# Kernel tuning notes

Measured on AMD Instinct MI355X. Metric: run time of the kernel, lower is better.

The kernel has to match this reference:

```python
import jax, jax.numpy as jnp
import numpy as np

EPS = 1e-6
NH, DK, DV = 4, 32, 32

def _ln2d(x, w, b):
    # LayerNorm2d: normalize over channel dim (dim=1), biased variance
    mu = jnp.mean(x, axis=1, keepdims=True)
    var = jnp.mean((x - mu) ** 2, axis=1, keepdims=True)
    y = (x - mu) / jnp.sqrt(var + EPS)
    return w[None, :, None, None] * y + b[None, :, None, None]

def _c1x1(w, x):
    # 1x1 conv == per-pixel matmul: w [out,in], x [B,C,H,W]
    return jnp.einsum('oc,bchw->bohw', w, x)

def _shifts(x, r):
    # All (2r+1)^2 zero-padded spatial shifts, row-major (dy,dx) like nn.Unfold.
    B, C, H, W = x.shape
    xp = jnp.pad(x, ((0, 0), (0, 0), (r, r), (r, r)))
    return jnp.stack([xp[:, :, dy:dy + H, dx:dx + W]
                      for dy in range(2 * r + 1) for dx in range(2 * r + 1)], axis=0)

def _local_attn(q, k, v, kernel):
    # Correlation-pyramid local attention: per-pixel q.k over kxk window of k,
    # softmax over window (temperature sqrt(d_k)), weighted sum of v window
    # (weights shared across channels, per ChannelAttention).
    B, _, H, W = q.shape
    r = (kernel - 1) // 2
    K2 = kernel * kernel
    qh = q.reshape(B, NH, DK, H, W)
    ks = _shifts(k, r).reshape(K2, B, NH, DK, H, W)
    corr = jnp.einsum('bncyx,jbncyx->jbnyx', qh, ks)            # [K2,B,NH,H,W]
    attn = jax.nn.softmax(corr / jnp.sqrt(jnp.float32(DK)), axis=0)
    vs = _shifts(v, r).reshape(K2, B, NH, DV, H, W)
    out = jnp.einsum('jbnyx,jbncyx->bncyx', attn, vs)
    return out.reshape(B, NH * DV, H, W)

def _mha(q, k, v, kernel, wq, wk, wv, fc, lnw, lnb):
    resid = q
    heads = _local_attn(_c1x1(wq, q), _c1x1(wk, k), _c1x1(wv, v), kernel)
    out = _c1x1(fc, heads) + resid   # residual BEFORE LN (per source)
    return _ln2d(out, lnw, lnb)

def _ffn(x, w1, b1, w2, b2, lnw, lnb):
    h = jax.nn.relu(_c1x1(w1, x) + b1[None, :, None, None])
    y = _c1x1(w2, h) + b2[None, :, None, None]
    return _ln2d(y, lnw, lnb) + x    # LN BEFORE residual add (per source)

def setup_inputs():
    key = jax.random.key(0)
    ks = jax.random.split(key, 24)
    B, C, H, W = 4, 128, 96, 96
    s = (2.0 / C) ** 0.5
    f = jnp.float32
    return {
        'input1': jax.random.normal(ks[0], (B, C, H, W), f),
        'input2': jax.random.normal(ks[1], (B, C, H, W), f),
        'wq_s': jax.random.normal(ks[2], (NH * DK, C), f) * s,
        'wk_s': jax.random.normal(ks[3], (NH * DK, C), f) * s,
        'wv_s': jax.random.normal(ks[4], (NH * DV, C), f) * s,
        'fc_s': jax.random.normal(ks[5], (C, NH * DV), f) * s,
        'lnw_s': jnp.ones((C,), f),
        'lnb_s': jnp.zeros((C,), f),
        'wq_c': jax.random.normal(ks[6], (NH * DK, C), f) * s,
        'wk_c': jax.random.normal(ks[7], (NH * DK, C), f) * s,
        'wv_c': jax.random.normal(ks[8], (NH * DV, C), f) * s,
        'fc_c': jax.random.normal(ks[9], (C, NH * DV), f) * s,
        'lnw_c': jnp.ones((C,), f),
        'lnb_c': jnp.zeros((C,), f),
        'w1': jax.random.normal(ks[10], (C, C), f) * s,
        'b1': jnp.zeros((C,), f),
        'w2': jax.random.normal(ks[11], (C, C), f) * s,
        'b2': jnp.zeros((C,), f),
        'lnw_f': jnp.ones((C,), f),
        'lnb_f': jnp.zeros((C,), f),
        'kernel': 5,
        'pad': 2,
    }

def reference(input1, input2, wq_s, wk_s, wv_s, fc_s, lnw_s, lnb_s,
              wq_c, wk_c, wv_c, fc_c, lnw_c, lnb_c,
              w1, b1, w2, b2, lnw_f, lnb_f, kernel, pad):
    slf1 = _mha(input1, input1, input1, kernel, wq_s, wk_s, wv_s, fc_s, lnw_s, lnb_s)
    slf2 = _mha(input2, input2, input2, kernel, wq_s, wk_s, wv_s, fc_s, lnw_s, lnb_s)
    crs1 = _mha(slf1, slf2, slf2, kernel, wq_c, wk_c, wv_c, fc_c, lnw_c, lnb_c)
    crs2 = _mha(slf2, slf1, slf1, kernel, wq_c, wk_c, wv_c, fc_c, lnw_c, lnb_c)
    out1 = _ffn(crs1, w1, b1, w2, b2, lnw_f, lnb_f)
    out2 = _ffn(crs2, w1, b1, w2, b2, lnw_f, lnb_f)
    return (out1, out2)
```

## Files before the change

### kernel.cpp

```cpp
#include <hip/hip_runtime.h>
#include <hip/hip_bf16.h>

typedef _Float16 h16;
typedef __attribute__((ext_vector_type(8))) _Float16 f16x8v;
typedef __attribute__((ext_vector_type(2))) _Float16 h2v;
typedef __attribute__((ext_vector_type(4))) float f32x4;
#define DI __device__ __forceinline__

constexpr int CH = 128;
constexpr int HH = 96, WW = 96;
constexpr int HW = HH * WW;
constexpr int NB = 4;
constexpr int NPIX = NB * HW;
constexpr int LDT = 136;
constexpr size_t HP = (size_t)NPIX * 32;
constexpr int GH = NPIX / 64;
constexpr int TY = 4, TX = 32;
constexpr int HYH = TY + 4, HXH = TX + 4;
constexpr int LDC = 40;
constexpr int ATB = NPIX / (TY * TX) * 4;

struct __attribute__((aligned(16))) h16x8 { h16 h[8]; };
struct Set { h16 *q, *k, *v; };

DI float h2f(h16 x) { return (float)x; }
DI h16   f2h(float x) { return (h16)x; }


DI void stage_x_cl(const h16* __restrict__ src, int ldx, h16* xl, int t) {
    #pragma unroll
    for (int i = 0; i < 4; ++i) {
        int id = t + 256 * i, px = id >> 4, cc = (id & 15) * 8;
        *reinterpret_cast<f16x8v*>(&xl[px * LDT + cc]) =
            *reinterpret_cast<const f16x8v*>(&src[(size_t)px * ldx + cc]);
    }
}

DI void stage_x_pl(const float* __restrict__ src, h16* xl, int t) {
    #pragma unroll
    for (int i = 0; i < 8; ++i) {
        int id = t + 256 * i, c = id >> 4, p4 = (id & 15) * 4;
        float4 v = *reinterpret_cast<const float4*>(&src[(size_t)c * HW + p4]);
        xl[(p4 + 0) * LDT + c] = f2h(v.x);
        xl[(p4 + 1) * LDT + c] = f2h(v.y);
        xl[(p4 + 2) * LDT + c] = f2h(v.z);
        xl[(p4 + 3) * LDT + c] = f2h(v.w);
    }
}

DI void stage_x_hm(const h16* __restrict__ Tq, h16* xl, int p0, int t) {
    const int px = t >> 2, c8 = (t & 3) * 8;
    #pragma unroll
    for (int h = 0; h < 4; ++h)
        *reinterpret_cast<f16x8v*>(&xl[px * LDT + h * 32 + c8]) =
            *reinterpret_cast<const f16x8v*>(&Tq[(size_t)h * HP + (size_t)(p0 + px) * 32 + c8]);
}

DI void stage_w(const float* __restrict__ w, h16* wl, int t) {
    #pragma unroll
    for (int i = 0; i < 8; ++i) {
        int id = t + 256 * i, o = id >> 4, cc = (id & 15) * 8;
        float4 a = *reinterpret_cast<const float4*>(&w[o * CH + cc]);
        float4 b = *reinterpret_cast<const float4*>(&w[o * CH + cc + 4]);
        h16x8 tmp;
        tmp.h[0] = f2h(a.x); tmp.h[1] = f2h(a.y); tmp.h[2] = f2h(a.z); tmp.h[3] = f2h(a.w);
        tmp.h[4] = f2h(b.x); tmp.h[5] = f2h(b.y); tmp.h[6] = f2h(b.z); tmp.h[7] = f2h(b.w);
        *reinterpret_cast<f16x8v*>(&wl[o * LDT + cc]) = *reinterpret_cast<const f16x8v*>(&tmp);
    }
}

DI void gemm64(const h16* xl, const h16* wl, int w, int l, f32x4* acc) {
    const int s = l & 15, g = l >> 4;
    #pragma unroll
    for (int ks = 0; ks < 4; ++ks) {
        f16x8v a = *reinterpret_cast<const f16x8v*>(&xl[(16 * w + s) * LDT + ks * 32 + g * 8]);
        #pragma unroll
        for (int n = 0; n < 8; ++n) {
            f16x8v b = *reinterpret_cast<const f16x8v*>(&wl[(16 * n + s) * LDT + ks * 32 + g * 8]);
            acc[n] = __builtin_amdgcn_mfma_f32_16x16x32_f16(a, b, acc[n], 0, 0, 0);
        }
    }
}

DI void qkv_epi(const f32x4* acc, h16* comp, int p0, int w, int l) {
    const int s = l & 15, g = l >> 4;
    #pragma unroll
    for (int n = 0; n < 8; ++n) {
        const int o = 16 * n + s, head = o >> 5, ch = o & 31;
        h16* pl = comp + (size_t)head * HP;
        #pragma unroll
        for (int j = 0; j < 4; ++j) {
            int px = 16 * w + 4 * g + j;
            pl[(size_t)(p0 + px) * 32 + ch] = f2h(acc[n][j]);
        }
    }
}

__global__ __launch_bounds__(256, 2)
void qkv_self_b(const float* __restrict__ x0, const float* __restrict__ x1,
                const float* __restrict__ w0, const float* __restrict__ w1_,
                const float* __restrict__ w2_, Set sA, Set sB) {
    __shared__ h16 xl[64 * LDT];
    __shared__ h16 wl[CH * LDT];
    const int bid = blockIdx.x, half = bid / GH, p0 = (bid % GH) * 64;
    const float* xv = half ? x1 : x0;
    Set S = half ? sB : sA;
    const int t = threadIdx.x;
    const int b = p0 / HW, hw0 = p0 % HW;
    stage_x_pl(xv + (size_t)b * CH * HW + hw0, xl, t);
    const int w = t >> 6, l = t & 63;
    #pragma unroll
    for (int m = 0; m < 3; ++m) {
        const float* wm = (m == 0) ? w0 : ((m == 1) ? w1_ : w2_);
        h16* comp = (m == 0) ? S.q : ((m == 1) ? S.k : S.v);
        __syncthreads();
        stage_w(wm, wl, t);
        __syncthreads();
        f32x4 acc[8];
        #pragma unroll
        for (int n = 0; n < 8; ++n) acc[n] = {0.f, 0.f, 0.f, 0.f};
        gemm64(xl, wl, w, l, acc);
        qkv_epi(acc, comp, p0, w, l);
    }
}

__global__ __launch_bounds__(256, 2)
void qkv_cross_b(const h16* __restrict__ xa, const h16* __restrict__ xb,
                 const float* __restrict__ wq, const float* __restrict__ wk,
                 const float* __restrict__ wv, Set c1, Set c2) {
    __shared__ h16 xl[64 * LDT];
    __shared__ h16 wl[CH * LDT];
    const int bid = blockIdx.x, half = bid / GH, p0 = (bid % GH) * 64;
    const h16* xq  = half ? xb : xa;
    const h16* xkv = half ? xa : xb;
    Set S = half ? c2 : c1;
    const int t = threadIdx.x;
    const int w = t >> 6, l = t & 63;

    stage_x_cl(xq + (size_t)p0 * CH, CH, xl, t);
    stage_w(wq, wl, t);
    __syncthreads();
    {
        f32x4 acc[8];
        #pragma unroll
        for (int n = 0; n < 8; ++n) acc[n] = {0.f, 0.f, 0.f, 0.f};
        gemm64(xl, wl, w, l, acc);
        qkv_epi(acc, S.q, p0, w, l);
    }
    __syncthreads();
    stage_x_cl(xkv + (size_t)p0 * CH, CH, xl, t);
    stage_w(wk, wl, t);
    __syncthreads();
    {
        f32x4 acc[8];
        #pragma unroll
        for (int n = 0; n < 8; ++n) acc[n] = {0.f, 0.f, 0.f, 0.f};
        gemm64(xl, wl, w, l, acc);
        qkv_epi(acc, S.k, p0, w, l);
    }
    __syncthreads();
    stage_w(wv, wl, t);
    __syncthreads();
    {
        f32x4 acc[8];
        #pragma unroll
        for (int n = 0; n < 8; ++n) acc[n] = {0.f, 0.f, 0.f, 0.f};
        gemm64(xl, wl, w, l, acc);
        qkv_epi(acc, S.v, p0, w, l);
    }
}

__global__ __launch_bounds__(256)
void attn5b(Set s0, Set s1) {
    __shared__ h16 kv[HYH * HXH * LDC];
    const int bid = blockIdx.x, setId = bid / ATB, id = bid - setId * ATB;
    Set S = setId ? s1 : s0;
    const int n = id & 3, tile = id >> 2;
    const int img = tile / 72, rem = tile % 72, tr = rem / 3, tc = rem % 3;
    const int y0 = tr * TY, x0 = tc * TX;
    const int t = threadIdx.x;
    const int p = t >> 1, half = t & 1, ch16 = half * 16;
    const int ty = p >> 5, tx = p & 31;
    h16* Qh = S.q + (size_t)n * HP;
    const h16* Kh = S.k + (size_t)n * HP;
    const h16* Vh = S.v + (size_t)n * HP;
    const int gp = img * HW + (y0 + ty) * WW + (x0 + tx);
    h16* qp = Qh + (size_t)gp * 32 + ch16;

    f16x8v q0 = *reinterpret_cast<const f16x8v*>(qp);
    f16x8v q1 = *reinterpret_cast<const f16x8v*>(qp + 8);
    {
        const h16 sc = (h16)0.17677669529663689f;
        #pragma unroll
        for (int e = 0; e < 8; ++e) { q0[e] *= sc; q1[e] *= sc; }
    }

    #pragma unroll
    for (int i = 0; i < 5; ++i) {
        int id2 = t + 256 * i;
        if (id2 < 1152) {
            int r = id2 / 144, c = id2 - r * 144, px = c >> 2, c8 = (c & 3) * 8;
            int y = y0 + r - 2, x = x0 + px - 2;
            f16x8v v = {0, 0, 0, 0, 0, 0, 0, 0};
            if ((unsigned)y < (unsigned)HH && (unsigned)x < (unsigned)WW)
                v = *reinterpret_cast<const f16x8v*>(&Kh[((size_t)(img * HW + y * WW + x)) * 32 + c8]);
            *reinterpret_cast<f16x8v*>(&kv[(r * HXH + px) * LDC + c8]) = v;
        }
    }
    __syncthreads();

    float corr[25];
    #pragma unroll
    for (int dy = 0; dy < 5; ++dy)
        #pragma unroll
        for (int dx = 0; dx < 5; ++dx) {
            const h16* kp = &kv[((ty + dy) * HXH + tx + dx) * LDC + ch16];
            f16x8v k0 = *reinterpret_cast<const f16x8v*>(kp);
            f16x8v k1 = *reinterpret_cast<const f16x8v*>(kp + 8);
            float s;
#if __has_builtin(__builtin_amdgcn_fdot2)
            s = __builtin_amdgcn_fdot2(h2v{q0[0], q0[1]}, h2v{k0[0], k0[1]}, 0.f, false);
            s = __builtin_amdgcn_fdot2(h2v{q0[2], q0[3]}, h2v{k0[2], k0[3]}, s, false);
            s = __builtin_amdgcn_fdot2(h2v{q0[4], q0[5]}, h2v{k0[4], k0[5]}, s, false);
            s = __builtin_amdgcn_fdot2(h2v{q0[6], q0[7]}, h2v{k0[6], k0[7]}, s, false);
            s = __builtin_amdgcn_fdot2(h2v{q1[0], q1[1]}, h2v{k1[0], k1[1]}, s, false);
            s = __builtin_amdgcn_fdot2(h2v{q1[2], q1[3]}, h2v{k1[2], k1[3]}, s, false);
            s = __builtin_amdgcn_fdot2(h2v{q1[4], q1[5]}, h2v{k1[4], k1[5]}, s, false);
            s = __builtin_amdgcn_fdot2(h2v{q1[6], q1[7]}, h2v{k1[6], k1[7]}, s, false);
#else
            s = 0.f;
            #pragma unroll
            for (int e = 0; e < 8; ++e) s += h2f(q0[e]) * h2f(k0[e]);
            #pragma unroll
            for (int e = 0; e < 8; ++e) s += h2f(q1[e]) * h2f(k1[e]);
#endif
            s += __shfl_xor(s, 1);
            corr[dy * 5 + dx] = s;
        }

    float m = corr[0];
    #pragma unroll
    for (int j = 1; j < 25; ++j) m = fmaxf(m, corr[j]);
    float sum = 0.f;
    #pragma unroll
    for (int j = 0; j < 25; ++j) {
        float e = __expf(corr[j] - m);
        corr[j] = e; sum += e;
    }
    const float inv = 1.f / sum;

    __syncthreads();
    #pragma unroll
    for (int i = 0; i < 5; ++i) {
        int id2 = t + 256 * i;
        if (id2 < 1152) {
            int r = id2 / 144, c = id2 - r * 144, px = c >> 2, c8 = (c & 3) * 8;
            int y = y0 + r - 2, x = x0 + px - 2;
            f16x8v v = {0, 0, 0, 0, 0, 0, 0, 0};
            if ((unsigned)y < (unsigned)HH && (unsigned)x < (unsigned)WW)
                v = *reinterpret_cast<const f16x8v*>(&Vh[((size_t)(img * HW + y * WW + x)) * 32 + c8]);
            *reinterpret_cast<f16x8v*>(&kv[(r * HXH + px) * LDC + c8]) = v;
        }
    }
    __syncthreads();

    f16x8v o0 = {0, 0, 0, 0, 0, 0, 0, 0};
    f16x8v o1 = {0, 0, 0, 0, 0, 0, 0, 0};
    #pragma unroll
    for (int dy = 0; dy < 5; ++dy)
        #pragma unroll
        for (int dx = 0; dx < 5; ++dx) {
            const h16 ah = f2h(corr[dy * 5 + dx]);
            const f16x8v av = {ah, ah, ah, ah, ah, ah, ah, ah};
            const h16* vp = &kv[((ty + dy) * HXH + tx + dx) * LDC + ch16];
            f16x8v v0 = *reinterpret_cast<const f16x8v*>(vp);
            f16x8v v1 = *reinterpret_cast<const f16x8v*>(vp + 8);
            o0 += av * v0;
            o1 += av * v1;
        }
    {
        const h16 ih = f2h(inv);
        const f16x8v iv = {ih, ih, ih, ih, ih, ih, ih, ih};
        o0 *= iv; o1 *= iv;
    }
    *reinterpret_cast<f16x8v*>(qp)     = o0;
    *reinterpret_cast<f16x8v*>(qp + 8) = o1;
}

template<bool RPLANAR>
__global__ __launch_bounds__(256, 2)
void fcln_b(const h16* __restrict__ t0, const h16* __restrict__ t1,
            const void* __restrict__ r0, const void* __restrict__ r1,
            const float* __restrict__ wfc, const float* __restrict__ gamma,
            const float* __restrict__ beta, h16* __restrict__ o0,
            h16* __restrict__ o1) {
    __shared__ h16 xl[64 * LDT];
    __shared__ h16 wl[CH * LDT];
    const int bid = blockIdx.x, half = bid / GH, p0 = (bid % GH) * 64;
    const h16* tin = half ? t1 : t0;
    const void* residv = half ? r1 : r0;
    h16* out = half ? o1 : o0;
    const int t = threadIdx.x;
    stage_x_hm(tin, xl, p0, t);
    stage_w(wfc, wl, t);
    __syncthreads();
    const int w = t >> 6, l = t & 63, s = l & 15, g = l >> 4;
    f32x4 acc[8];
    #pragma unroll
    for (int n = 0; n < 8; ++n) acc[n] = {0.f, 0.f, 0.f, 0.f};
    gemm64(xl, wl, w, l, acc);

    const int b = p0 / HW, hw0 = p0 % HW;
    float r[8][4];
    #pragma unroll
    for (int n = 0; n < 8; ++n) {
        const int o = 16 * n + s;
        #pragma unroll
        for (int j = 0; j < 4; ++j) {
            const int px = 16 * w + 4 * g + j;
            float rv;
            if (RPLANAR)
                rv = ((const float*)residv)[(size_t)b * CH * HW + (size_t)o * HW + hw0 + px];
            else
                rv = h2f(((const h16*)residv)[(size_t)(p0 + px) * CH + o]);
            r[n][j] = acc[n][j] + rv;
        }
    }
    float gm[8], bt[8];
    #pragma unroll
    for (int n = 0; n < 8; ++n) { gm[n] = gamma[16 * n + s]; bt[n] = beta[16 * n + s]; }
    #pragma unroll
    for (int j = 0; j < 4; ++j) {
        float sm = 0.f, sq = 0.f;
        #pragma unroll
        for (int n = 0; n < 8; ++n) { float v = r[n][j]; sm += v; sq += v * v; }
        sm += __shfl_xor(sm, 1); sq += __shfl_xor(sq, 1);
        sm += __shfl_xor(sm, 2); sq += __shfl_xor(sq, 2);
        sm += __shfl_xor(sm, 4); sq += __shfl_xor(sq, 4);
        sm += __shfl_xor(sm, 8); sq += __shfl_xor(sq, 8);
        const float mu = sm * (1.f / 128.f);
        const float var = sq * (1.f / 128.f) - mu * mu;
        const float rs = rsqrtf(var + 1e-6f);
        const int px = 16 * w + 4 * g + j;
        #pragma unroll
        for (int n = 0; n < 8; ++n) {
            const int o = 16 * n + s;
            out[(size_t)(p0 + px) * CH + o] = f2h(gm[n] * (r[n][j] - mu) * rs + bt[n]);
        }
    }
}

__global__ __launch_bounds__(256, 2)
void ffn_fused(const h16* __restrict__ y0, const h16* __restrict__ y1,
               const float* __restrict__ w1m, const float* __restrict__ b1v,
               const float* __restrict__ w2m, const float* __restrict__ b2v,
               const float* __restrict__ gamma, const float* __restrict__ beta,
               float* __restrict__ o0, float* __restrict__ o1) {
    __shared__ __align__(16) char smem[64 * LDT * 2 * 2 + CH * LDT * 2];
    h16*   xl = (h16*)smem;
    h16*   hl = (h16*)(smem + 64 * LDT * 2);
    h16*   wl = (h16*)(smem + 64 * LDT * 2 * 2);
    float* ll = (float*)(smem + 64 * LDT * 2 * 2);
    const int bid = blockIdx.x, half = bid / GH, p0 = (bid % GH) * 64;
    const h16* y = half ? y1 : y0;
    float* outp = half ? o1 : o0;
    const int t = threadIdx.x;
    stage_x_cl(y + (size_t)p0 * CH, CH, xl, t);
    stage_w(w1m, wl, t);
    __syncthreads();
    const int w = t >> 6, l = t & 63, s = l & 15, g = l >> 4;
    f32x4 acc[8];
    #pragma unroll
    for (int n = 0; n < 8; ++n) acc[n] = {0.f, 0.f, 0.f, 0.f};
    gemm64(xl, wl, w, l, acc);
    #pragma unroll
    for (int n = 0; n < 8; ++n) {
        const int o = 16 * n + s;
        const float bv = b1v[o];
        #pragma unroll
        for (int j = 0; j < 4; ++j) {
            const int px = 16 * w + 4 * g + j;
            hl[px * LDT + o] = f2h(fmaxf(acc[n][j] + bv, 0.f));
        }
    }
    __syncthreads();
    stage_w(w2m, wl, t);
    __syncthreads();
    f32x4 acc2[8];
    #pragma unroll
    for (int n = 0; n < 8; ++n) acc2[n] = {0.f, 0.f, 0.f, 0.f};
    gemm64(hl, wl, w, l, acc2);

    float gm[8], bt[8], r[8][4];
    #pragma unroll
    for (int n = 0; n < 8; ++n) {
        const int o = 16 * n + s;
        gm[n] = gamma[o]; bt[n] = beta[o];
        const float bv = b2v[o];
        #pragma unroll
        for (int j = 0; j < 4; ++j) r[n][j] = acc2[n][j] + bv;
    }
    float val[8][4];
    #pragma unroll
    for (int j = 0; j < 4; ++j) {
        float sm = 0.f, sq = 0.f;
        #pragma unroll
        for (int n = 0; n < 8; ++n) { float v = r[n][j]; sm += v; sq += v * v; }
        sm += __shfl_xor(sm, 1); sq += __shfl_xor(sq, 1);
        sm += __shfl_xor(sm, 2); sq += __shfl_xor(sq, 2);
        sm += __shfl_xor(sm, 4); sq += __shfl_xor(sq, 4);
        sm += __shfl_xor(sm, 8); sq += __shfl_xor(sq, 8);
        const float mu = sm * (1.f / 128.f);
        const float var = sq * (1.f / 128.f) - mu * mu;
        const float rs = rsqrtf(var + 1e-6f);
        const int px = 16 * w + 4 * g + j;
        #pragma unroll
        for (int n = 0; n < 8; ++n) {
            const int o = 16 * n + s;
            val[n][j] = gm[n] * (r[n][j] - mu) * rs + bt[n]
                      + h2f(xl[px * LDT + o]);
        }
    }
    __syncthreads();
    #pragma unroll
    for (int n = 0; n < 8; ++n) {
        const int o = 16 * n + s;
        #pragma unroll
        for (int j = 0; j < 4; ++j) ll[o * 65 + 16 * w + 4 * g + j] = val[n][j];
    }
    __syncthreads();
    const int b = p0 / HW, hw0 = p0 % HW;
    #pragma unroll
    for (int i = 0; i < 8; ++i) {
        int id = t + 256 * i, c = id >> 4, p4 = (id & 15) * 4;
        float4 v = { ll[c * 65 + p4], ll[c * 65 + p4 + 1],
                     ll[c * 65 + p4 + 2], ll[c * 65 + p4 + 3] };
        *reinterpret_cast<float4*>(&outp[(size_t)b * CH * HW + (size_t)c * HW + hw0 + p4]) = v;
    }
}

extern "C" void kernel_launch(void* const* d_in, const int* in_sizes, int n_in,
                              void* d_out, int out_size, void* d_ws, size_t ws_size,
                              hipStream_t stream) {
    (void)in_sizes; (void)n_in; (void)out_size; (void)ws_size;
    const float* in1  = (const float*)d_in[0];
    const float* in2  = (const float*)d_in[1];
    const float* wq_s = (const float*)d_in[2];
    const float* wk_s = (const float*)d_in[3];
    const float* wv_s = (const float*)d_in[4];
    const float* fc_s = (const float*)d_in[5];
    const float* lnw_s= (const float*)d_in[6];
    const float* lnb_s= (const float*)d_in[7];
    const float* wq_c = (const float*)d_in[8];
    const float* wk_c = (const float*)d_in[9];
    const float* wv_c = (const float*)d_in[10];
    const float* fc_c = (const float*)d_in[11];
    const float* lnw_c= (const float*)d_in[12];
    const float* lnb_c= (const float*)d_in[13];
    const float* w1   = (const float*)d_in[14];
    const float* b1   = (const float*)d_in[15];
    const float* w2   = (const float*)d_in[16];
    const float* b2   = (const float*)d_in[17];
    const float* lnw_f= (const float*)d_in[18];
    const float* lnb_f= (const float*)d_in[19];

    const size_t BUF  = (size_t)NPIX * CH;
    const size_t BUFB = BUF * 2;
    char* ws = (char*)d_ws;
    h16* W0 = (h16*)(ws + 0 * BUFB);
    h16* W1 = (h16*)(ws + 1 * BUFB);
    h16* W2 = (h16*)(ws + 2 * BUFB);
    h16* W3 = (h16*)(ws + 3 * BUFB);
    h16* D0 = (h16*)d_out;
    h16* D1 = (h16*)((char*)d_out + 1 * BUFB);
    h16* D2 = (h16*)((char*)d_out + 2 * BUFB);
    h16* D3 = (h16*)((char*)d_out + 3 * BUFB);
    float* out1 = (float*)d_out;
    float* out2 = (float*)d_out + BUF;

    const dim3 B(256), BA(256);

    Set SA = {W0, W1, W2};
    Set SB = {W3, D0, D1};
    h16* X1 = D2;
    h16* X2 = D3;

    qkv_self_b<<<dim3(2 * GH), B, 0, stream>>>(in1, in2, wq_s, wk_s, wv_s, SA, SB);
    attn5b<<<dim3(2 * ATB), BA, 0, stream>>>(SA, SB);
    fcln_b<true><<<dim3(2 * GH), B, 0, stream>>>(SA.q, SB.q, in1, in2,
                                                 fc_s, lnw_s, lnb_s, X1, X2);

    Set C1 = {W0, W1, W2};
    Set C2 = {W3, D0, D1};
    qkv_cross_b<<<dim3(2 * GH), B, 0, stream>>>(X1, X2, wq_c, wk_c, wv_c, C1, C2);
    attn5b<<<dim3(2 * ATB), BA, 0, stream>>>(C1, C2);
    h16* Y1 = W1;
    h16* Y2 = W2;
    fcln_b<false><<<dim3(2 * GH), B, 0, stream>>>(C1.q, C2.q, X1, X2,
                                                  fc_c, lnw_c, lnb_c, Y1, Y2);

    ffn_fused<<<dim3(2 * GH), B, 0, stream>>>(Y1, Y2, w1, b1, w2, b2,
                                              lnw_f, lnb_f, out1, out2);
}
```

Measured before the change: 162.9 us.

## Fuse self-attn fc+LN into cross QKV projection and cross fc+LN into FFN

Merges the self-attention output projection, residual and LayerNorm with the cross-attention QKV projections into one kernel. Each block processes both streams for its 64 pixels, so the normalized X1/X2 tiles stay in shared memory and feed the Q/K/V GEMMs without a reload. The cross-attention fc+LN is likewise folded into the FFN kernel, cutting the pipeline from seven launches to five and removing global round trips of intermediates. In exchange the fused kernel launches half as many blocks, each with more shared memory and longer serial work, which may lower occupancy and parallelism.

```diff
diff --git a/kernel.cpp b/kernel.cpp
--- a/kernel.cpp
+++ b/kernel.cpp
@@ -93,6 +93,25 @@
             int px = 16 * w + 4 * g + j;
             pl[(size_t)(p0 + px) * 32 + ch] = f2h(acc[n][j]);
         }
+    }
+}
+
+DI void ln128(float r[8][4], const float* gm, const float* bt, float val[8][4]) {
+    #pragma unroll
+    for (int j = 0; j < 4; ++j) {
+        float sm = 0.f, sq = 0.f;
+        #pragma unroll
+        for (int n = 0; n < 8; ++n) { float v = r[n][j]; sm += v; sq += v * v; }
+        sm += __shfl_xor(sm, 1); sq += __shfl_xor(sq, 1);
+        sm += __shfl_xor(sm, 2); sq += __shfl_xor(sq, 2);
+        sm += __shfl_xor(sm, 4); sq += __shfl_xor(sq, 4);
+        sm += __shfl_xor(sm, 8); sq += __shfl_xor(sq, 8);
+        const float mu = sm * (1.f / 128.f);
+        const float var = sq * (1.f / 128.f) - mu * mu;
+        const float rs = rsqrtf(var + 1e-6f);
+        #pragma unroll
+        for (int n = 0; n < 8; ++n)
+            val[n][j] = gm[n] * (r[n][j] - mu) * rs + bt[n];
     }
 }
 
@@ -121,52 +140,6 @@
         for (int n = 0; n < 8; ++n) acc[n] = {0.f, 0.f, 0.f, 0.f};
         gemm64(xl, wl, w, l, acc);
         qkv_epi(acc, comp, p0, w, l);
-    }
-}
-
-__global__ __launch_bounds__(256, 2)
-void qkv_cross_b(const h16* __restrict__ xa, const h16* __restrict__ xb,
-                 const float* __restrict__ wq, const float* __restrict__ wk,
-                 const float* __restrict__ wv, Set c1, Set c2) {
-    __shared__ h16 xl[64 * LDT];
-    __shared__ h16 wl[CH * LDT];
-    const int bid = blockIdx.x, half = bid / GH, p0 = (bid % GH) * 64;
-    const h16* xq  = half ? xb : xa;
-    const h16* xkv = half ? xa : xb;
-    Set S = half ? c2 : c1;
-    const int t = threadIdx.x;
-    const int w = t >> 6, l = t & 63;
-
-    stage_x_cl(xq + (size_t)p0 * CH, CH, xl, t);
-    stage_w(wq, wl, t);
-    __syncthreads();
-    {
-        f32x4 acc[8];
-        #pragma unroll
-        for (int n = 0; n < 8; ++n) acc[n] = {0.f, 0.f, 0.f, 0.f};
-        gemm64(xl, wl, w, l, acc);
-        qkv_epi(acc, S.q, p0, w, l);
-    }
-    __syncthreads();
-    stage_x_cl(xkv + (size_t)p0 * CH, CH, xl, t);
-    stage_w(wk, wl, t);
-    __syncthreads();
-    {
-        f32x4 acc[8];
-        #pragma unroll
-        for (int n = 0; n < 8; ++n) acc[n] = {0.f, 0.f, 0.f, 0.f};
-        gemm64(xl, wl, w, l, acc);
-        qkv_epi(acc, S.k, p0, w, l);
-    }
-    __syncthreads();
-    stage_w(wv, wl, t);
-    __syncthreads();
-    {
-        f32x4 acc[8];
-        #pragma unroll
-        for (int n = 0; n < 8; ++n) acc[n] = {0.f, 0.f, 0.f, 0.f};
-        gemm64(xl, wl, w, l, acc);
-        qkv_epi(acc, S.v, p0, w, l);
     }
 }
 
@@ -287,146 +260,251 @@
     *reinterpret_cast<f16x8v*>(qp + 8) = o1;
 }
 
-template<bool RPLANAR>
 __global__ __launch_bounds__(256, 2)
-void fcln_b(const h16* __restrict__ t0, const h16* __restrict__ t1,
-            const void* __restrict__ r0, const void* __restrict__ r1,
-            const float* __restrict__ wfc, const float* __restrict__ gamma,
-            const float* __restrict__ beta, h16* __restrict__ o0,
-            h16* __restrict__ o1) {
-    __shared__ h16 xl[64 * LDT];
+void fcx_b(const h16* __restrict__ tA, const h16* __restrict__ tB,
+           const float* __restrict__ in1, const float* __restrict__ in2,
+           const float* __restrict__ wfc, const float* __restrict__ gamma,
+           const float* __restrict__ beta,
+           const float* __restrict__ wq, const float* __restrict__ wk,
+           const float* __restrict__ wv,
+           h16* __restrict__ x1g, h16* __restrict__ x2g, Set c1, Set c2) {
+    __shared__ h16 xA[64 * LDT];
+    __shared__ h16 xB[64 * LDT];
     __shared__ h16 wl[CH * LDT];
-    const int bid = blockIdx.x, half = bid / GH, p0 = (bid % GH) * 64;
-    const h16* tin = half ? t1 : t0;
-    const void* residv = half ? r1 : r0;
-    h16* out = half ? o1 : o0;
-    const int t = threadIdx.x;
-    stage_x_hm(tin, xl, p0, t);
+    const int t = threadIdx.x, p0 = blockIdx.x * 64;
+    const int w = t >> 6, l = t & 63, s = l & 15, g4 = l >> 4;
+    const int b = p0 / HW, hw0 = p0 % HW;
+
+    stage_x_hm(tA, xA, p0, t);
+    stage_x_hm(tB, xB, p0, t);
     stage_w(wfc, wl, t);
     __syncthreads();
-    const int w = t >> 6, l = t & 63, s = l & 15, g = l >> 4;
-    f32x4 acc[8];
-    #pragma unroll
-    for (int n = 0; n < 8; ++n) acc[n] = {0.f, 0.f, 0.f, 0.f};
-    gemm64(xl, wl, w, l, acc);
-
-    const int b = p0 / HW, hw0 = p0 % HW;
-    float r[8][4];
+
+    float gm[8], bt[8];
+    #pragma unroll
+    for (int n = 0; n < 8; ++n) { gm[n] = gamma[16 * n + s]; bt[n] = beta[16 * n + s]; }
+
+    h16 vA[8][4], vB[8][4];
+    {
+        f32x4 acc[8];
+        #pragma unroll
+        for (int n = 0; n < 8; ++n) acc[n] = {0.f, 0.f, 0.f, 0.f};
+        gemm64(xA, wl, w, l, acc);
+        float r[8][4], val[8][4];
+        #pragma unroll
+        for (int n = 0; n < 8; ++n) {
+            const int o = 16 * n + s;
+            #pragma unroll
+            for (int j = 0; j < 4; ++j) {
+                const int px = 16 * w + 4 * g4 + j;
+                r[n][j] = acc[n][j] +
+                    in1[(size_t)b * CH * HW + (size_t)o * HW + hw0 + px];
+            }
+        }
+        ln128(r, gm, bt, val);
+        #pragma unroll
+        for (int n = 0; n < 8; ++n)
+            #pragma unroll
+            for (int j = 0; j < 4; ++j) vA[n][j] = f2h(val[n][j]);
+    }
+    {
+        f32x4 acc[8];
+        #pragma unroll
+        for (int n = 0; n < 8; ++n) acc[n] = {0.f, 0.f, 0.f, 0.f};
+        gemm64(xB, wl, w, l, acc);
+        float r[8][4], val[8][4];
+        #pragma unroll
+        for (int n = 0; n < 8; ++n) {
+            const int o = 16 * n + s;
+            #pragma unroll
+            for (int j = 0; j < 4; ++j) {
+                const int px = 16 * w + 4 * g4 + j;
+                r[n][j] = acc[n][j] +
+                    in2[(size_t)b * CH * HW + (size_t)o * HW + hw0 + px];
+            }
+        }
+        ln128(r, gm, bt, val);
+        #pragma unroll
+        for (int n = 0; n < 8; ++n)
+            #pragma unroll
+            for (int j = 0; j < 4; ++j) vB[n][j] = f2h(val[n][j]);
+    }
+    __syncthreads();
     #pragma unroll
     for (int n = 0; n < 8; ++n) {
         const int o = 16 * n + s;
         #pragma unroll
         for (int j = 0; j < 4; ++j) {
-            const int px = 16 * w + 4 * g + j;
-            float rv;
-            if (RPLANAR)
-                rv = ((const float*)residv)[(size_t)b * CH * HW + (size_t)o * HW + hw0 + px];
-            else
-                rv = h2f(((const h16*)residv)[(size_t)(p0 + px) * CH + o]);
-            r[n][j] = acc[n][j] + rv;
-        }
-    }
-    float gm[8], bt[8];
-    #pragma unroll
-    for (int n = 0; n < 8; ++n) { gm[n] = gamma[16 * n + s]; bt[n] = beta[16 * n + s]; }
-    #pragma unroll
-    for (int j = 0; j < 4; ++j) {
-        float sm = 0.f, sq = 0.f;
-        #pragma unroll
-        for (int n = 0; n < 8; ++n) { float v = r[n][j]; sm += v; sq += v * v; }
-        sm += __shfl_xor(sm, 1); sq += __shfl_xor(sq, 1);
-        sm += __shfl_xor(sm, 2); sq += __shfl_xor(sq, 2);
-        sm += __shfl_xor(sm, 4); sq += __shfl_xor(sq, 4);
-        sm += __shfl_xor(sm, 8); sq += __shfl_xor(sq, 8);
-        const float mu = sm * (1.f / 128.f);
-        const float var = sq * (1.f / 128.f) - mu * mu;
-        const float rs = rsqrtf(var + 1e-6f);
-        const int px = 16 * w + 4 * g + j;
-        #pragma unroll
-        for (int n = 0; n < 8; ++n) {
-            const int o = 16 * n + s;
-            out[(size_t)(p0 + px) * CH + o] = f2h(gm[n] * (r[n][j] - mu) * rs + bt[n]);
-        }
+            const int px = 16 * w + 4 * g4 + j;
+            xA[px * LDT + o] = vA[n][j];
+            xB[px * LDT + o] = vB[n][j];
+            x1g[(size_t)(p0 + px) * CH + o] = vA[n][j];
+            x2g[(size_t)(p0 + px) * CH + o] = vB[n][j];
+        }
+    }
+    __syncthreads();
+
+    stage_w(wq, wl, t);
+    __syncthreads();
+    {
+        f32x4 acc[8];
+        #pragma unroll
+        for (int n = 0; n < 8; ++n) acc[n] = {0.f, 0.f, 0.f, 0.f};
+        gemm64(xA, wl, w, l, acc);
+        qkv_epi(acc, c1.q, p0, w, l);
+    }
+    {
+        f32x4 acc[8];
+        #pragma unroll
+        for (int n = 0; n < 8; ++n) acc[n] = {0.f, 0.f, 0.f, 0.f};
+        gemm64(xB, wl, w, l, acc);
+        qkv_epi(acc, c2.q, p0, w, l);
+    }
+    __syncthreads();
+    stage_w(wk, wl, t);
+    __syncthreads();
+    {
+        f32x4 acc[8];
+        #pragma unroll
+        for (int n = 0; n < 8; ++n) acc[n] = {0.f, 0.f, 0.f, 0.f};
+        gemm64(xB, wl, w, l, acc);
+        qkv_epi(acc, c1.k, p0, w, l);
+    }
+    {
+        f32x4 acc[8];
+        #pragma unroll
+        for (int n = 0; n < 8; ++n) acc[n] = {0.f, 0.f, 0.f, 0.f};
+        gemm64(xA, wl, w, l, acc);
+        qkv_epi(acc, c2.k, p0, w, l);
+    }
+    __syncthreads();
+    stage_w(wv, wl, t);
+    __syncthreads();
+    {
+        f32x4 acc[8];
+        #pragma unroll
+        for (int n = 0; n < 8; ++n) acc[n] = {0.f, 0.f, 0.f, 0.f};
+        gemm64(xB, wl, w, l, acc);
+        qkv_epi(acc, c1.v, p0, w, l);
+    }
+    {
+        f32x4 acc[8];
+        #pragma unroll
+        for (int n = 0; n < 8; ++n) acc[n] = {0.f, 0.f, 0.f, 0.f};
+        gemm64(xA, wl, w, l, acc);
+        qkv_epi(acc, c2.v, p0, w, l);
     }
 }
 
 __global__ __launch_bounds__(256, 2)
-void ffn_fused(const h16* __restrict__ y0, const h16* __restrict__ y1,
-               const float* __restrict__ w1m, const float* __restrict__ b1v,
-               const float* __restrict__ w2m, const float* __restrict__ b2v,
-               const float* __restrict__ gamma, const float* __restrict__ beta,
-               float* __restrict__ o0, float* __restrict__ o1) {
+void ffn_ln_b(const h16* __restrict__ t0, const h16* __restrict__ t1,
+              const h16* __restrict__ x0, const h16* __restrict__ x1,
+              const float* __restrict__ wfc, const float* __restrict__ gc,
+              const float* __restrict__ bc,
+              const float* __restrict__ w1m, const float* __restrict__ b1v,
+              const float* __restrict__ w2m, const float* __restrict__ b2v,
+              const float* __restrict__ gf, const float* __restrict__ bf,
+              float* __restrict__ o0, float* __restrict__ o1) {
     __shared__ __align__(16) char smem[64 * LDT * 2 * 2 + CH * LDT * 2];
     h16*   xl = (h16*)smem;
-    h16*   hl = (h16*)(smem + 64 * LDT * 2);
+    h16*   yl = (h16*)(smem + 64 * LDT * 2);
     h16*   wl = (h16*)(smem + 64 * LDT * 2 * 2);
     float* ll = (float*)(smem + 64 * LDT * 2 * 2);
     const int bid = blockIdx.x, half = bid / GH, p0 = (bid % GH) * 64;
-    const h16* y = half ? y1 : y0;
+    const h16* tin = half ? t1 : t0;
+    const h16* xg  = half ? x1 : x0;
     float* outp = half ? o1 : o0;
     const int t = threadIdx.x;
-    stage_x_cl(y + (size_t)p0 * CH, CH, xl, t);
-    stage_w(w1m, wl, t);
-    __syncthreads();
-    const int w = t >> 6, l = t & 63, s = l & 15, g = l >> 4;
-    f32x4 acc[8];
-    #pragma unroll
-    for (int n = 0; n < 8; ++n) acc[n] = {0.f, 0.f, 0.f, 0.f};
-    gemm64(xl, wl, w, l, acc);
+    const int w = t >> 6, l = t & 63, s = l & 15, g4 = l >> 4;
+
+    stage_x_hm(tin, xl, p0, t);
+    stage_w(wfc, wl, t);
+    __syncthreads();
+
+    h16 yv[8][4];
+    {
+        f32x4 acc[8];
+        #pragma unroll
+        for (int n = 0; n < 8; ++n) acc[n] = {0.f, 0.f, 0.f, 0.f};
+        gemm64(xl, wl, w, l, acc);
+        float gm[8], bt[8], r[8][4], val[8][4];
+        #pragma unroll
+        for (int n = 0; n < 8; ++n) { gm[n] = gc[16 * n + s]; bt[n] = bc[16 * n + s]; }
+        #pragma unroll
+        for (int n = 0; n < 8; ++n) {
+            const int o = 16 * n + s;
+            #pragma unroll
+            for (int j = 0; j < 4; ++j) {
+                const int px = 16 * w + 4 * g4 + j;
+                r[n][j] = acc[n][j] + h2f(xg[(size_t)(p0 + px) * CH + o]);
+            }
+        }
+        ln128(r, gm, bt, val);
+        #pragma unroll
+        for (int n = 0; n < 8; ++n)
+            #pragma unroll
+            for (int j = 0; j < 4; ++j) yv[n][j] = f2h(val[n][j]);
+    }
+    __syncthreads();
     #pragma unroll
     for (int n = 0; n < 8; ++n) {
         const int o = 16 * n + s;
-        const float bv = b1v[o];
-        #pragma unroll
-        for (int j = 0; j < 4; ++j) {
-            const int px = 16 * w + 4 * g + j;
-            hl[px * LDT + o] = f2h(fmaxf(acc[n][j] + bv, 0.f));
+        #pragma unroll
+        for (int j = 0; j < 4; ++j)
+            yl[(16 * w + 4 * g4 + j) * LDT + o] = yv[n][j];
+    }
+    stage_w(w1m, wl, t);
+    __syncthreads();
+
+    {
+        f32x4 acc[8];
+        #pragma unroll
+        for (int n = 0; n < 8; ++n) acc[n] = {0.f, 0.f, 0.f, 0.f};
+        gemm64(yl, wl, w, l, acc);
+        #pragma unroll
+        for (int n = 0; n < 8; ++n) {
+            const int o = 16 * n + s;
+            const float bv = b1v[o];
+            #pragma unroll
+            for (int j = 0; j < 4; ++j)
+                xl[(16 * w + 4 * g4 + j) * LDT + o] = f2h(fmaxf(acc[n][j] + bv, 0.f));
         }
     }
     __syncthreads();
     stage_w(w2m, wl, t);
     __syncthreads();
-    f32x4 acc2[8];
-    #pragma unroll
-    for (int n = 0; n < 8; ++n) acc2[n] = {0.f, 0.f, 0.f, 0.f};
-    gemm64(hl, wl, w, l, acc2);
-
-    float gm[8], bt[8], r[8][4];
+
+    float val[8][4];
+    {
+        f32x4 acc[8];
+        #pragma unroll
+        for (int n = 0; n < 8; ++n) acc[n] = {0.f, 0.f, 0.f, 0.f};
+        gemm64(xl, wl, w, l, acc);
+        float gm[8], bt[8], r[8][4];
+        #pragma unroll
+        for (int n = 0; n < 8; ++n) { gm[n] = gf[16 * n + s]; bt[n] = bf[16 * n + s]; }
+        #pragma unroll
+        for (int n = 0; n < 8; ++n) {
+            const int o = 16 * n + s;
+            const float bv = b2v[o];
+            #pragma unroll
+            for (int j = 0; j < 4; ++j) r[n][j] = acc[n][j] + bv;
+        }
+        ln128(r, gm, bt, val);
+        #pragma unroll
+        for (int n = 0; n < 8; ++n) {
+            const int o = 16 * n + s;
+            #pragma unroll
+            for (int j = 0; j < 4; ++j)
+                val[n][j] += h2f(yl[(16 * w + 4 * g4 + j) * LDT + o]);
+        }
+    }
+    __syncthreads();
     #pragma unroll
     for (int n = 0; n < 8; ++n) {
         const int o = 16 * n + s;
-        gm[n] = gamma[o]; bt[n] = beta[o];
-        const float bv = b2v[o];
-        #pragma unroll
-        for (int j = 0; j < 4; ++j) r[n][j] = acc2[n][j] + bv;
-    }
-    float val[8][4];
-    #pragma unroll
-    for (int j = 0; j < 4; ++j) {
-        float sm = 0.f, sq = 0.f;
-        #pragma unroll
-        for (int n = 0; n < 8; ++n) { float v = r[n][j]; sm += v; sq += v * v; }
-        sm += __shfl_xor(sm, 1); sq += __shfl_xor(sq, 1);
-        sm += __shfl_xor(sm, 2); sq += __shfl_xor(sq, 2);
-        sm += __shfl_xor(sm, 4); sq += __shfl_xor(sq, 4);
-        sm += __shfl_xor(sm, 8); sq += __shfl_xor(sq, 8);
-        const float mu = sm * (1.f / 128.f);
-        const float var = sq * (1.f / 128.f) - mu * mu;
-        const float rs = rsqrtf(var + 1e-6f);
-        const int px = 16 * w + 4 * g + j;
-        #pragma unroll
-        for (int n = 0; n < 8; ++n) {
-            const int o = 16 * n + s;
-            val[n][j] = gm[n] * (r[n][j] - mu) * rs + bt[n]
-                      + h2f(xl[px * LDT + o]);
-        }
-    }
-    __syncthreads();
-    #pragma unroll
-    for (int n = 0; n < 8; ++n) {
-        const int o = 16 * n + s;
-        #pragma unroll
-        for (int j = 0; j < 4; ++j) ll[o * 65 + 16 * w + 4 * g + j] = val[n][j];
+        #pragma unroll
+        for (int j = 0; j < 4; ++j) ll[o * 65 + 16 * w + 4 * g4 + j] = val[n][j];
     }
     __syncthreads();
     const int b = p0 / HW, hw0 = p0 % HW;
@@ -478,27 +556,23 @@
     float* out1 = (float*)d_out;
     float* out2 = (float*)d_out + BUF;
 
-    const dim3 B(256), BA(256);
-
-    Set SA = {W0, W1, W2};
-    Set SB = {W3, D0, D1};
-    h16* X1 = D2;
-    h16* X2 = D3;
+    const dim3 B(256);
+
+    Set SA = {W0, D0, D1};
+    Set SB = {W1, D2, D3};
+    h16* X1 = W2;
+    h16* X2 = W3;
+    Set C1 = {W0, D0, D1};
+    Set C2 = {W1, D2, D3};
 
     qkv_self_b<<<dim3(2 * GH), B, 0, stream>>>(in1, in2, wq_s, wk_s, wv_s, SA, SB);
-    attn5b<<<dim3(2 * ATB), BA, 0, stream>>>(SA, SB);
-    fcln_b<true><<<dim3(2 * GH), B, 0, stream>>>(SA.q, SB.q, in1, in2,
-                                                 fc_s, lnw_s, lnb_s, X1, X2);
-
-    Set C1 = {W0, W1, W2};
-    Set C2 = {W3, D0, D1};
-    qkv_cross_b<<<dim3(2 * GH), B, 0, stream>>>(X1, X2, wq_c, wk_c, wv_c, C1, C2);
-    attn5b<<<dim3(2 * ATB), BA, 0, stream>>>(C1, C2);
-    h16* Y1 = W1;
-    h16* Y2 = W2;
-    fcln_b<false><<<dim3(2 * GH), B, 0, stream>>>(C1.q, C2.q, X1, X2,
-                                                  fc_c, lnw_c, lnb_c, Y1, Y2);
-
-    ffn_fused<<<dim3(2 * GH), B, 0, stream>>>(Y1, Y2, w1, b1, w2, b2,
-                                              lnw_f, lnb_f, out1, out2);
-}
+    attn5b<<<dim3(2 * ATB), B, 0, stream>>>(SA, SB);
+    fcx_b<<<dim3(GH), B, 0, stream>>>(SA.q, SB.q, in1, in2,
+                                      fc_s, lnw_s, lnb_s,
+                                      wq_c, wk_c, wv_c, X1, X2, C1, C2);
+    attn5b<<<dim3(2 * ATB), B, 0, stream>>>(C1, C2);
+    ffn_ln_b<<<dim3(2 * GH), B, 0, stream>>>(C1.q, C2.q, X1, X2,
+                                             fc_c, lnw_c, lnb_c,
+                                             w1, b1, w2, b2, lnw_f, lnb_f,
+                                             out1, out2);
+}
```

New measurement: 156.9 us. 3.7% less time.
